# Performance work log

Measured on AMD Instinct MI355X. Metric: run time of the kernel, lower is better.

Reference implementation:

```python
import jax, jax.numpy as jnp
import numpy as np

N_NODES = 100_000
N_EDGES = 3_200_000
HIDDEN = 16


def setup_inputs() -> dict:
    key = jax.random.key(0)
    k1, k2, k3, k4 = jax.random.split(key, 4)
    x = jax.random.normal(k1, (N_NODES, 3), dtype=jnp.float32)
    edge_index = jax.random.randint(k2, (2, N_EDGES), 0, N_NODES, dtype=jnp.int32)
    # Glorot-style init for the two GCN layers (PyG GCNConv: lin weight + bias)
    W1 = jax.random.normal(k3, (3, HIDDEN), dtype=jnp.float32) * (1.0 / np.sqrt(3.0))
    b1 = jnp.zeros((HIDDEN,), dtype=jnp.float32)
    W2 = jax.random.normal(k4, (HIDDEN, 1), dtype=jnp.float32) * (1.0 / np.sqrt(HIDDEN))
    b2 = jnp.zeros((1,), dtype=jnp.float32)
    return {"x": x, "edge_index": edge_index, "W1": W1, "b1": b1, "W2": W2, "b2": b2}


def reference(x, edge_index, W1, b1, W2, b2):
    n = x.shape[0]  # static under jit
    # GCNConv default: add self-loops, symmetric degree normalization
    self_loop = jnp.arange(n, dtype=edge_index.dtype)
    src = jnp.concatenate([edge_index[0], self_loop])
    dst = jnp.concatenate([edge_index[1], self_loop])
    deg = jax.ops.segment_sum(jnp.ones_like(src, dtype=x.dtype), dst, num_segments=n)
    inv_sqrt_deg = jnp.where(deg > 0, jax.lax.rsqrt(jnp.maximum(deg, 1.0)), 0.0)
    norm = inv_sqrt_deg[src] * inv_sqrt_deg[dst]  # [E+N]

    def gcn_conv(h, W, b):
        h = h @ W  # linear transform first (cheaper: small out dim)
        msg = norm[:, None] * h[src]  # gather + scale
        return jax.ops.segment_sum(msg, dst, num_segments=n) + b  # scatter-add

    h = jax.nn.relu(gcn_conv(x, W1, b1))
    out = gcn_conv(h, W2, b2)
    return out.squeeze(-1)  # [N]
```

## Files before the change

### kernel.cpp

```cpp
#include <hip/hip_runtime.h>

#define HIDDEN 16
#define FB 128
#define FB_SHIFT 7
#define NBK_MAX 4096
#define FCHUNK 8192
#define FTH 512
#define CB 1024
#define CB_SHIFT 10
#define NCB_MAX 512
#define CHUNK 4096
#define SPL 8
#define BT 1024


__global__ __launch_bounds__(FTH) void
k_histf(const int* __restrict__ dst, int e, int nbk, int nchunk,
        unsigned int* __restrict__ hcT) {
    __shared__ unsigned int h[NBK_MAX];
    for (int i = threadIdx.x; i < nbk; i += FTH) h[i] = 0u;
    __syncthreads();
    int start = blockIdx.x * FCHUNK;
    int end = min(start + FCHUNK, e);
    for (int i = start + threadIdx.x; i < end; i += FTH)
        atomicAdd(&h[((unsigned)dst[i]) >> FB_SHIFT], 1u);
    __syncthreads();
    for (int j = threadIdx.x; j < nbk; j += FTH)
        hcT[(size_t)j * nchunk + blockIdx.x] = h[j];
}

__global__ void k_scanf(unsigned int* __restrict__ hcT,
                        unsigned int* __restrict__ cntc, int nchunk) {
    __shared__ unsigned int ts[256];
    __shared__ unsigned int carry;
    int b = blockIdx.x, t = threadIdx.x;
    if (t == 0) carry = 0u;
    __syncthreads();
    size_t row = (size_t)b * nchunk;
    for (int t0 = 0; t0 < nchunk; t0 += 256) {
        int i = t0 + t;
        unsigned int v = (i < nchunk) ? hcT[row + i] : 0u;
        ts[t] = v;
        __syncthreads();
        for (int off = 1; off < 256; off <<= 1) {
            unsigned int u = (t >= off) ? ts[t - off] : 0u;
            __syncthreads();
            ts[t] += u;
            __syncthreads();
        }
        if (i < nchunk) hcT[row + i] = carry + ts[t] - v;
        __syncthreads();
        if (t == 0) carry += ts[255];
        __syncthreads();
    }
    if (t == 0) cntc[b] = carry;
}

__global__ __launch_bounds__(1024) void
k_scanb(const unsigned int* __restrict__ cntc, int nbk,
        unsigned int* __restrict__ basec,
        unsigned int* __restrict__ rowptr, int n, unsigned int e) {
    __shared__ unsigned int tsum[1024];
    int t = threadIdx.x;
    int K = (nbk + 1023) / 1024;
    unsigned int s = 0;
    for (int k = 0; k < K; k++) {
        int i = t * K + k;
        if (i < nbk) s += cntc[i];
    }
    tsum[t] = s;
    __syncthreads();
    for (int off = 1; off < 1024; off <<= 1) {
        unsigned int v = (t >= off) ? tsum[t - off] : 0u;
        __syncthreads();
        tsum[t] += v;
        __syncthreads();
    }
    unsigned int run = (t == 0) ? 0u : tsum[t - 1];
    for (int k = 0; k < K; k++) {
        int i = t * K + k;
        if (i < nbk) { basec[i] = run; run += cntc[i]; }
    }
    if (t == 1023) basec[nbk] = tsum[1023];
    if (t == 0) rowptr[n] = e;
}

__global__ __launch_bounds__(FTH) void
k_fillf(const int* __restrict__ src, const int* __restrict__ dst,
        int e, int nbk, int nchunk,
        const unsigned int* __restrict__ basec,
        const unsigned int* __restrict__ hcT,
        unsigned int* __restrict__ tmp) {
    __shared__ unsigned int h[NBK_MAX];
    __shared__ unsigned int lb[NBK_MAX];
    for (int j = threadIdx.x; j < nbk; j += FTH) {
        lb[j] = basec[j] + hcT[(size_t)j * nchunk + blockIdx.x];
        h[j] = 0u;
    }
    __syncthreads();
    int start = blockIdx.x * FCHUNK;
    int end = min(start + FCHUNK, e);
    for (int i = start + threadIdx.x; i < end; i += FTH) {
        unsigned int d = (unsigned)dst[i];
        unsigned int s = (unsigned)src[i];
        unsigned int b = d >> FB_SHIFT;
        unsigned int r = atomicAdd(&h[b], 1u);
        tmp[lb[b] + r] = (s << FB_SHIFT) | (d & (FB - 1u));
    }
}

__global__ __launch_bounds__(256) void
k_sortN(const unsigned int* __restrict__ tmp,
        const unsigned int* __restrict__ basec,
        const float* __restrict__ x,
        unsigned int* __restrict__ rowptr, unsigned int* __restrict__ tmp2,
        float4* __restrict__ xs4, int n) {
    __shared__ unsigned int cnt[FB];
    __shared__ unsigned int sc[FB];
    __shared__ unsigned int cur[FB];
    int t = threadIdx.x, b = blockIdx.x;
    unsigned int s = basec[b], endp = basec[b + 1];
    if (t < FB) cnt[t] = 0u;
    __syncthreads();
    for (unsigned int i = s + t; i < endp; i += 256)
        atomicAdd(&cnt[tmp[i] & (FB - 1u)], 1u);
    __syncthreads();
    if (t < FB) sc[t] = cnt[t];
    __syncthreads();
    for (int off = 1; off < FB; off <<= 1) {
        unsigned int v = (t < FB && t >= off) ? sc[t - off] : 0u;
        __syncthreads();
        if (t < FB && t >= off) sc[t] += v;
        __syncthreads();
    }
    if (t < FB) {
        unsigned int excl = sc[t] - cnt[t];
        cur[t] = s + excl;
        int node = (b << FB_SHIFT) + t;
        if (node < n) {
            rowptr[node] = s + excl;
            float iv = rsqrtf((float)(1u + cnt[t]));
            xs4[node] = make_float4(x[3 * node] * iv, x[3 * node + 1] * iv,
                                    x[3 * node + 2] * iv, iv);
        }
    }
    __syncthreads();
    for (unsigned int i = s + t; i < endp; i += 256) {
        unsigned int rec = tmp[i];
        unsigned int r = atomicAdd(&cur[rec & (FB - 1u)], 1u);
        tmp2[r] = rec >> FB_SHIFT;
    }
}

__global__ void k_s1(const unsigned int* __restrict__ rowptr,
                     const unsigned int* __restrict__ tmp2,
                     const float4* __restrict__ xs4,
                     const float* __restrict__ W1, const float* __restrict__ b1,
                     const float* __restrict__ W2, const float* __restrict__ b2,
                     float* __restrict__ t2s, float* __restrict__ out, int n) {
    int gid = blockIdx.x * blockDim.x + threadIdx.x;
    int i = gid >> 1, h = gid & 1;
    bool valid = (i < n);
    unsigned int s = 0, epos = 0;
    if (valid) { s = rowptr[i]; epos = rowptr[i + 1]; }
    unsigned int half = (epos - s) >> 1;
    unsigned int b0 = h ? s + half : s;
    unsigned int b1r = h ? epos : s + half;
    float v0 = 0.f, v1 = 0.f, v2 = 0.f;
    unsigned int j = b0;
    for (; j + 4 <= b1r; j += 4) {
        unsigned a0 = tmp2[j], a1 = tmp2[j + 1], a2 = tmp2[j + 2], a3 = tmp2[j + 3];
        float4 p0 = xs4[a0], p1 = xs4[a1], p2 = xs4[a2], p3 = xs4[a3];
        v0 += (p0.x + p1.x) + (p2.x + p3.x);
        v1 += (p0.y + p1.y) + (p2.y + p3.y);
        v2 += (p0.z + p1.z) + (p2.z + p3.z);
    }
    for (; j < b1r; j++) {
        float4 p = xs4[tmp2[j]];
        v0 += p.x; v1 += p.y; v2 += p.z;
    }
    v0 += __shfl_xor(v0, 1);
    v1 += __shfl_xor(v1, 1);
    v2 += __shfl_xor(v2, 1);
    if (valid && h == 0) {
        float4 me = xs4[i];
        float iv = me.w;
        v0 = (v0 + me.x) * iv;
        v1 = (v1 + me.y) * iv;
        v2 = (v2 + me.z) * iv;
        float acc = 0.f;
#pragma unroll
        for (int k = 0; k < HIDDEN; k++) {
            float hh = fmaxf(fmaf(v0, W1[k], fmaf(v1, W1[HIDDEN + k],
                            fmaf(v2, W1[2 * HIDDEN + k], b1[k]))), 0.f);
            acc += hh * W2[k];
        }
        t2s[i] = acc * iv;
        out[i] = b2[0] + acc * iv * iv;
    }
}

__global__ void k_s2(const unsigned int* __restrict__ rowptr,
                     const unsigned int* __restrict__ tmp2,
                     const float* __restrict__ t2s, const float4* __restrict__ xs4,
                     float* __restrict__ out, int n) {
    int gid = blockIdx.x * blockDim.x + threadIdx.x;
    int i = gid >> 1, h = gid & 1;
    bool valid = (i < n);
    unsigned int s = 0, epos = 0;
    if (valid) { s = rowptr[i]; epos = rowptr[i + 1]; }
    unsigned int half = (epos - s) >> 1;
    unsigned int b0 = h ? s + half : s;
    unsigned int b1r = h ? epos : s + half;
    float v = 0.f;
    unsigned int j = b0;
    for (; j + 4 <= b1r; j += 4) {
        unsigned a0 = tmp2[j], a1 = tmp2[j + 1], a2 = tmp2[j + 2], a3 = tmp2[j + 3];
        v += (t2s[a0] + t2s[a1]) + (t2s[a2] + t2s[a3]);
    }
    for (; j < b1r; j++) v += t2s[tmp2[j]];
    v += __shfl_xor(v, 1);
    if (valid && h == 0) out[i] += v * xs4[i].w;
}


__global__ void k_zero(unsigned int* a, int na) {
    int i = blockIdx.x * blockDim.x + threadIdx.x;
    if (i < na) a[i] = 0u;
}
__global__ void k_hist_c(const int* __restrict__ dst, int e, int ncb, int nchunk,
                         unsigned int* __restrict__ cntc,
                         unsigned int* __restrict__ hcT) {
    __shared__ unsigned int h[NCB_MAX];
    for (int i = threadIdx.x; i < ncb; i += blockDim.x) h[i] = 0u;
    __syncthreads();
    int start = blockIdx.x * CHUNK;
    int end = min(start + CHUNK, e);
    for (int i = start + threadIdx.x; i < end; i += 256)
        atomicAdd(&h[((unsigned)dst[i]) >> CB_SHIFT], 1u);
    __syncthreads();
    for (int j = threadIdx.x; j < ncb; j += blockDim.x) {
        hcT[(size_t)j * nchunk + blockIdx.x] = h[j];
        if (h[j]) atomicAdd(&cntc[j], h[j]);
    }
}
__global__ void k_scan(const unsigned int* __restrict__ cnt, int nb,
                       unsigned int* __restrict__ base) {
    __shared__ unsigned int tsum[256];
    int t = threadIdx.x;
    int K = (nb + 255) / 256;
    unsigned int s = 0;
    for (int k = 0; k < K; k++) {
        int i = t * K + k;
        if (i < nb) s += cnt[i];
    }
    tsum[t] = s;
    __syncthreads();
    for (int off = 1; off < 256; off <<= 1) {
        unsigned int v = (t >= off) ? tsum[t - off] : 0u;
        __syncthreads();
        tsum[t] += v;
        __syncthreads();
    }
    unsigned int run = (t == 0) ? 0u : tsum[t - 1];
    for (int k = 0; k < K; k++) {
        int i = t * K + k;
        if (i < nb) { base[i] = run; run += cnt[i]; }
    }
}
__global__ void k_scanc(const unsigned int* __restrict__ hcT,
                        const unsigned int* __restrict__ basec,
                        unsigned int* __restrict__ lbasec, int nchunk) {
    __shared__ unsigned int ts[256];
    __shared__ unsigned int carry;
    int b = blockIdx.x, t = threadIdx.x;
    if (t == 0) carry = basec[b];
    __syncthreads();
    for (int t0 = 0; t0 < nchunk; t0 += 256) {
        int i = t0 + t;
        unsigned int v = (i < nchunk) ? hcT[(size_t)b * nchunk + i] : 0u;
        ts[t] = v;
        __syncthreads();
        for (int off = 1; off < 256; off <<= 1) {
            unsigned int u = (t >= off) ? ts[t - off] : 0u;
            __syncthreads();
            ts[t] += u;
            __syncthreads();
        }
        if (i < nchunk) lbasec[(size_t)b * nchunk + i] = carry + ts[t] - v;
        __syncthreads();
        if (t == 0) carry += ts[255];
        __syncthreads();
    }
}
__global__ void k_fill_c(const int* __restrict__ src, const int* __restrict__ dst,
                         int e, int ncb, int nchunk,
                         const unsigned int* __restrict__ lbasec,
                         unsigned int* __restrict__ tmp) {
    __shared__ unsigned int h[NCB_MAX];
    __shared__ unsigned int lb[NCB_MAX];
    for (int j = threadIdx.x; j < ncb; j += blockDim.x) {
        lb[j] = lbasec[(size_t)j * nchunk + blockIdx.x];
        h[j] = 0u;
    }
    __syncthreads();
    int start = blockIdx.x * CHUNK;
    int end = min(start + CHUNK, e);
    for (int i = start + threadIdx.x; i < end; i += 256) {
        unsigned int d = (unsigned)dst[i];
        unsigned int b = d >> CB_SHIFT;
        unsigned int r = atomicAdd(&h[b], 1u);
        tmp[lb[b] + r] = (((unsigned)src[i]) << CB_SHIFT) | (d & (CB - 1u));
    }
}
__global__ __launch_bounds__(BT) void
k_deg_split(const unsigned int* __restrict__ tmp, const unsigned int* __restrict__ basec,
            const unsigned int* __restrict__ cntc, unsigned int* __restrict__ deg, int n) {
    __shared__ unsigned int degl[CB];
    int t = threadIdx.x;
    degl[t] = 0u;
    __syncthreads();
    int b = blockIdx.x / SPL, sl = blockIdx.x % SPL;
    unsigned int s = basec[b], m = cntc[b];
    for (unsigned int i = sl * BT + t; i < m; i += SPL * BT)
        atomicAdd(&degl[tmp[s + i] & (CB - 1u)], 1u);
    __syncthreads();
    int node = b * CB + t;
    unsigned int c = degl[t];
    if (node < n && c) atomicAdd(&deg[node], c);
}
__global__ void k_inv_s(const unsigned int* __restrict__ deg, const float* __restrict__ x,
                        float4* __restrict__ xs4, int n) {
    int i = blockIdx.x * blockDim.x + threadIdx.x;
    if (i >= n) return;
    float iv = rsqrtf((float)(deg[i] + 1u));
    xs4[i] = make_float4(x[3 * i] * iv, x[3 * i + 1] * iv, x[3 * i + 2] * iv, iv);
}
__global__ __launch_bounds__(BT) void
k_s1_split(const unsigned int* __restrict__ tmp, const unsigned int* __restrict__ basec,
           const unsigned int* __restrict__ cntc, const float4* __restrict__ xs4,
           float* __restrict__ agg0, float* __restrict__ agg1, float* __restrict__ agg2, int n) {
    __shared__ float a0[CB], a1[CB], a2[CB];
    int t = threadIdx.x;
    a0[t] = 0.f; a1[t] = 0.f; a2[t] = 0.f;
    __syncthreads();
    int b = blockIdx.x / SPL, sl = blockIdx.x % SPL;
    unsigned int s = basec[b], m = cntc[b];
    for (unsigned int i = sl * BT + t; i < m; i += SPL * BT) {
        unsigned rec = tmp[s + i];
        float4 v = xs4[rec >> CB_SHIFT];
        unsigned dl = rec & (CB - 1u);
        atomicAdd(&a0[dl], v.x); atomicAdd(&a1[dl], v.y); atomicAdd(&a2[dl], v.z);
    }
    __syncthreads();
    int node = b * CB + t;
    if (node < n) {
        if (a0[t] != 0.f) atomicAdd(&agg0[node], a0[t]);
        if (a1[t] != 0.f) atomicAdd(&agg1[node], a1[t]);
        if (a2[t] != 0.f) atomicAdd(&agg2[node], a2[t]);
    }
}
__global__ void k_epi_s(const float* __restrict__ agg0, const float* __restrict__ agg1,
                        const float* __restrict__ agg2, const float4* __restrict__ xs4,
                        const float* __restrict__ W1, const float* __restrict__ b1,
                        const float* __restrict__ W2, const float* __restrict__ b2,
                        float* __restrict__ t2s, float* __restrict__ out, int n) {
    int i = blockIdx.x * blockDim.x + threadIdx.x;
    if (i >= n) return;
    float4 xv = xs4[i];
    float iv = xv.w;
    float v0 = iv * (agg0[i] + xv.x), v1 = iv * (agg1[i] + xv.y), v2 = iv * (agg2[i] + xv.z);
    float acc = 0.f;
#pragma unroll
    for (int j = 0; j < HIDDEN; j++) {
        float h = fmaxf(fmaf(v0, W1[j], fmaf(v1, W1[HIDDEN + j],
                       fmaf(v2, W1[2 * HIDDEN + j], b1[j]))), 0.f);
        acc += h * W2[j];
    }
    t2s[i] = acc * iv;
    out[i] = b2[0] + acc * iv * iv;
}
__global__ __launch_bounds__(BT) void
k_s2_split(const unsigned int* __restrict__ tmp, const unsigned int* __restrict__ basec,
           const unsigned int* __restrict__ cntc, const float* __restrict__ t2s,
           const float4* __restrict__ xs4, float* __restrict__ out, int n) {
    __shared__ float o[CB];
    int t = threadIdx.x;
    o[t] = 0.f;
    __syncthreads();
    int b = blockIdx.x / SPL, sl = blockIdx.x % SPL;
    unsigned int s = basec[b], m = cntc[b];
    for (unsigned int i = sl * BT + t; i < m; i += SPL * BT) {
        unsigned rec = tmp[s + i];
        atomicAdd(&o[rec & (CB - 1u)], t2s[rec >> CB_SHIFT]);
    }
    __syncthreads();
    int node = b * CB + t;
    if (node < n && o[t] != 0.f) atomicAdd(&out[node], o[t] * xs4[node].w);
}


extern "C" void kernel_launch(void* const* d_in, const int* in_sizes, int n_in,
                              void* d_out, int out_size, void* d_ws, size_t ws_size,
                              hipStream_t stream) {
    const float* x  = (const float*)d_in[0];
    const int*   ei = (const int*)d_in[1];
    const float* W1 = (const float*)d_in[2];
    const float* b1 = (const float*)d_in[3];
    const float* W2 = (const float*)d_in[4];
    const float* b2 = (const float*)d_in[5];
    float* out = (float*)d_out;

    int n = in_sizes[0] / 3;
    int e = in_sizes[1] / 2;
    const int* src = ei;
    const int* dst = ei + e;
    const int B = 256;

    int nbk = (n + FB - 1) / FB;
    int nchunkf = (e + FCHUNK - 1) / FCHUNK;
    int gridN2 = (2 * n + B - 1) / B;

    size_t needf = (size_t)n * 16 + (size_t)n * 4 + (size_t)(n + 1) * 4
                 + (size_t)(2 * nbk + 1) * 4 + (size_t)nbk * nchunkf * 4
                 + (size_t)e * 8 + 64;

    if (nbk <= NBK_MAX && n < (1 << 25) && ws_size >= needf) {
        float4* xs4 = (float4*)d_ws;
        float* t2s = (float*)(xs4 + n);
        unsigned int* rowptr = (unsigned int*)(t2s + n);
        unsigned int* cntc   = rowptr + (n + 1);
        unsigned int* basec  = cntc + nbk;
        unsigned int* hcT    = basec + nbk + 1;
        unsigned int* tmp    = hcT + (size_t)nbk * nchunkf;
        unsigned int* tmp2   = tmp + e;

        k_histf<<<nchunkf, FTH, 0, stream>>>(dst, e, nbk, nchunkf, hcT);
        k_scanf<<<nbk, 256, 0, stream>>>(hcT, cntc, nchunkf);
        k_scanb<<<1, 1024, 0, stream>>>(cntc, nbk, basec, rowptr, n, (unsigned)e);
        k_fillf<<<nchunkf, FTH, 0, stream>>>(src, dst, e, nbk, nchunkf, basec, hcT, tmp);
        k_sortN<<<nbk, 256, 0, stream>>>(tmp, basec, x, rowptr, tmp2, xs4, n);
        k_s1<<<gridN2, B, 0, stream>>>(rowptr, tmp2, xs4, W1, b1, W2, b2, t2s, out, n);
        k_s2<<<gridN2, B, 0, stream>>>(rowptr, tmp2, t2s, xs4, out, n);
    } else {
        int ncb = (n + CB - 1) / CB;
        int gridE = (e + CHUNK - 1) / CHUNK;
        int gridN = (n + B - 1) / B;
        float4* xs4 = (float4*)d_ws;
        float* agg0 = (float*)(xs4 + n);
        float* agg1 = agg0 + n;
        float* agg2 = agg1 + n;
        unsigned int* deg = (unsigned int*)(agg2 + n);
        float* t2s = (float*)(deg + n);
        unsigned int* cntc   = (unsigned int*)(t2s + n);
        unsigned int* basec  = cntc + ncb;
        unsigned int* hcT    = basec + ncb;
        unsigned int* lbasec = hcT + (size_t)ncb * gridE;
        unsigned int* tmp    = lbasec + (size_t)ncb * gridE;

        k_zero<<<(4 * n + ncb + B - 1) / B, B, 0, stream>>>((unsigned int*)agg0, 4 * n);
        k_zero<<<(ncb + B - 1) / B, B, 0, stream>>>(cntc, ncb);
        k_hist_c<<<gridE, B, 0, stream>>>(dst, e, ncb, gridE, cntc, hcT);
        k_scan<<<1, B, 0, stream>>>(cntc, ncb, basec);
        k_scanc<<<ncb, B, 0, stream>>>(hcT, basec, lbasec, gridE);
        k_fill_c<<<gridE, B, 0, stream>>>(src, dst, e, ncb, gridE, lbasec, tmp);
        k_deg_split<<<ncb * SPL, BT, 0, stream>>>(tmp, basec, cntc, deg, n);
        k_inv_s<<<gridN, B, 0, stream>>>(deg, x, xs4, n);
        k_s1_split<<<ncb * SPL, BT, 0, stream>>>(tmp, basec, cntc, xs4, agg0, agg1, agg2, n);
        k_epi_s<<<gridN, B, 0, stream>>>(agg0, agg1, agg2, xs4, W1, b1, W2, b2, t2s, out, n);
        k_s2_split<<<ncb * SPL, BT, 0, stream>>>(tmp, basec, cntc, t2s, xs4, out, n);
    }
}
```

Baseline: 190.3 us.

## Use coarser 512-node buckets and reorder global scan in CSR build

Coarse bucket size grows from 128 to 512 nodes, cutting the bucket count and with it the per-chunk histogram matrix, the scan work and the shared-memory footprint of the histogram and fill kernels. Bucket totals are now gathered with global atomics during the histogram pass, so the global scan runs before the per-bucket chunk scan, which writes into a separate lbasec array. The histogram loop is also unrolled four ways. The trade-off is an extra zeroing launch, more work per bucket in the local sort (512 threads, longer scan), and fewer source bits left in the packed record (the node limit drops to 2^23).

Result: slower. 195.3 us (+2.6%).

```diff
diff --git a/kernel.cpp b/kernel.cpp
--- a/kernel.cpp
+++ b/kernel.cpp
@@ -1,11 +1,11 @@
 #include <hip/hip_runtime.h>
 
 #define HIDDEN 16
-#define FB 128
-#define FB_SHIFT 7
-#define NBK_MAX 4096
-#define FCHUNK 8192
-#define FTH 512
+#define MB 512
+#define MB_SHIFT 9
+#define NMB_MAX 1024
+#define MCHUNK 8192
+#define MTH 512
 #define CB 1024
 #define CB_SHIFT 10
 #define NCB_MAX 512
@@ -14,32 +14,76 @@
 #define BT 1024
 
 
-__global__ __launch_bounds__(FTH) void
-k_histf(const int* __restrict__ dst, int e, int nbk, int nchunk,
-        unsigned int* __restrict__ hcT) {
-    __shared__ unsigned int h[NBK_MAX];
-    for (int i = threadIdx.x; i < nbk; i += FTH) h[i] = 0u;
-    __syncthreads();
-    int start = blockIdx.x * FCHUNK;
-    int end = min(start + FCHUNK, e);
-    for (int i = start + threadIdx.x; i < end; i += FTH)
-        atomicAdd(&h[((unsigned)dst[i]) >> FB_SHIFT], 1u);
-    __syncthreads();
-    for (int j = threadIdx.x; j < nbk; j += FTH)
+__global__ void k_zerom(unsigned int* cntc, int nmb) {
+    int i = blockIdx.x * blockDim.x + threadIdx.x;
+    if (i < nmb) cntc[i] = 0u;
+}
+
+__global__ __launch_bounds__(MTH) void
+k_histm(const int* __restrict__ dst, int e, int nmb, int nchunk,
+        unsigned int* __restrict__ cntc, unsigned int* __restrict__ hcT) {
+    __shared__ unsigned int h[NMB_MAX];
+    for (int i = threadIdx.x; i < nmb; i += MTH) h[i] = 0u;
+    __syncthreads();
+    int start = blockIdx.x * MCHUNK;
+    int end = min(start + MCHUNK, e);
+    int i = start + threadIdx.x;
+    for (; i + 3 * MTH < end; i += 4 * MTH) {
+        unsigned d0 = dst[i], d1 = dst[i + MTH], d2 = dst[i + 2 * MTH], d3 = dst[i + 3 * MTH];
+        atomicAdd(&h[d0 >> MB_SHIFT], 1u);
+        atomicAdd(&h[d1 >> MB_SHIFT], 1u);
+        atomicAdd(&h[d2 >> MB_SHIFT], 1u);
+        atomicAdd(&h[d3 >> MB_SHIFT], 1u);
+    }
+    for (; i < end; i += MTH)
+        atomicAdd(&h[((unsigned)dst[i]) >> MB_SHIFT], 1u);
+    __syncthreads();
+    for (int j = threadIdx.x; j < nmb; j += MTH) {
         hcT[(size_t)j * nchunk + blockIdx.x] = h[j];
-}
-
-__global__ void k_scanf(unsigned int* __restrict__ hcT,
-                        unsigned int* __restrict__ cntc, int nchunk) {
+        if (h[j]) atomicAdd(&cntc[j], h[j]);
+    }
+}
+
+__global__ __launch_bounds__(1024) void
+k_scanm(const unsigned int* __restrict__ cntc, int nmb,
+        unsigned int* __restrict__ basec,
+        unsigned int* __restrict__ rowptr, int n, unsigned int e) {
+    __shared__ unsigned int tsum[1024];
+    int t = threadIdx.x;
+    int K = (nmb + 1023) / 1024;
+    unsigned int s = 0;
+    for (int k = 0; k < K; k++) {
+        int i = t * K + k;
+        if (i < nmb) s += cntc[i];
+    }
+    tsum[t] = s;
+    __syncthreads();
+    for (int off = 1; off < 1024; off <<= 1) {
+        unsigned int v = (t >= off) ? tsum[t - off] : 0u;
+        __syncthreads();
+        tsum[t] += v;
+        __syncthreads();
+    }
+    unsigned int run = (t == 0) ? 0u : tsum[t - 1];
+    for (int k = 0; k < K; k++) {
+        int i = t * K + k;
+        if (i < nmb) { basec[i] = run; run += cntc[i]; }
+    }
+    if (t == 1023) basec[nmb] = tsum[1023];
+    if (t == 0) rowptr[n] = e;
+}
+
+__global__ void k_scancm(const unsigned int* __restrict__ hcT,
+                         const unsigned int* __restrict__ basec,
+                         unsigned int* __restrict__ lbasec, int nchunk) {
     __shared__ unsigned int ts[256];
     __shared__ unsigned int carry;
     int b = blockIdx.x, t = threadIdx.x;
-    if (t == 0) carry = 0u;
-    __syncthreads();
-    size_t row = (size_t)b * nchunk;
+    if (t == 0) carry = basec[b];
+    __syncthreads();
     for (int t0 = 0; t0 < nchunk; t0 += 256) {
         int i = t0 + t;
-        unsigned int v = (i < nchunk) ? hcT[row + i] : 0u;
+        unsigned int v = (i < nchunk) ? hcT[(size_t)b * nchunk + i] : 0u;
         ts[t] = v;
         __syncthreads();
         for (int off = 1; off < 256; off <<= 1) {
@@ -48,107 +92,74 @@
             ts[t] += u;
             __syncthreads();
         }
-        if (i < nchunk) hcT[row + i] = carry + ts[t] - v;
+        if (i < nchunk) lbasec[(size_t)b * nchunk + i] = carry + ts[t] - v;
         __syncthreads();
         if (t == 0) carry += ts[255];
         __syncthreads();
     }
-    if (t == 0) cntc[b] = carry;
-}
-
-__global__ __launch_bounds__(1024) void
-k_scanb(const unsigned int* __restrict__ cntc, int nbk,
-        unsigned int* __restrict__ basec,
-        unsigned int* __restrict__ rowptr, int n, unsigned int e) {
-    __shared__ unsigned int tsum[1024];
-    int t = threadIdx.x;
-    int K = (nbk + 1023) / 1024;
-    unsigned int s = 0;
-    for (int k = 0; k < K; k++) {
-        int i = t * K + k;
-        if (i < nbk) s += cntc[i];
-    }
-    tsum[t] = s;
-    __syncthreads();
-    for (int off = 1; off < 1024; off <<= 1) {
-        unsigned int v = (t >= off) ? tsum[t - off] : 0u;
-        __syncthreads();
-        tsum[t] += v;
-        __syncthreads();
-    }
-    unsigned int run = (t == 0) ? 0u : tsum[t - 1];
-    for (int k = 0; k < K; k++) {
-        int i = t * K + k;
-        if (i < nbk) { basec[i] = run; run += cntc[i]; }
-    }
-    if (t == 1023) basec[nbk] = tsum[1023];
-    if (t == 0) rowptr[n] = e;
-}
-
-__global__ __launch_bounds__(FTH) void
-k_fillf(const int* __restrict__ src, const int* __restrict__ dst,
-        int e, int nbk, int nchunk,
-        const unsigned int* __restrict__ basec,
-        const unsigned int* __restrict__ hcT,
+}
+
+__global__ __launch_bounds__(MTH) void
+k_fillm(const int* __restrict__ src, const int* __restrict__ dst,
+        int e, int nmb, int nchunk,
+        const unsigned int* __restrict__ lbasec,
         unsigned int* __restrict__ tmp) {
-    __shared__ unsigned int h[NBK_MAX];
-    __shared__ unsigned int lb[NBK_MAX];
-    for (int j = threadIdx.x; j < nbk; j += FTH) {
-        lb[j] = basec[j] + hcT[(size_t)j * nchunk + blockIdx.x];
+    __shared__ unsigned int h[NMB_MAX];
+    __shared__ unsigned int lb[NMB_MAX];
+    for (int j = threadIdx.x; j < nmb; j += MTH) {
+        lb[j] = lbasec[(size_t)j * nchunk + blockIdx.x];
         h[j] = 0u;
     }
     __syncthreads();
-    int start = blockIdx.x * FCHUNK;
-    int end = min(start + FCHUNK, e);
-    for (int i = start + threadIdx.x; i < end; i += FTH) {
+    int start = blockIdx.x * MCHUNK;
+    int end = min(start + MCHUNK, e);
+    for (int i = start + threadIdx.x; i < end; i += MTH) {
         unsigned int d = (unsigned)dst[i];
         unsigned int s = (unsigned)src[i];
-        unsigned int b = d >> FB_SHIFT;
+        unsigned int b = d >> MB_SHIFT;
         unsigned int r = atomicAdd(&h[b], 1u);
-        tmp[lb[b] + r] = (s << FB_SHIFT) | (d & (FB - 1u));
-    }
-}
-
-__global__ __launch_bounds__(256) void
-k_sortN(const unsigned int* __restrict__ tmp,
+        tmp[lb[b] + r] = (s << MB_SHIFT) | (d & (MB - 1u));
+    }
+}
+
+__global__ __launch_bounds__(MB) void
+k_sortC(const unsigned int* __restrict__ tmp,
         const unsigned int* __restrict__ basec,
         const float* __restrict__ x,
         unsigned int* __restrict__ rowptr, unsigned int* __restrict__ tmp2,
         float4* __restrict__ xs4, int n) {
-    __shared__ unsigned int cnt[FB];
-    __shared__ unsigned int sc[FB];
-    __shared__ unsigned int cur[FB];
+    __shared__ unsigned int cnt[MB];
+    __shared__ unsigned int sc[MB];
+    __shared__ unsigned int cur[MB];
     int t = threadIdx.x, b = blockIdx.x;
     unsigned int s = basec[b], endp = basec[b + 1];
-    if (t < FB) cnt[t] = 0u;
-    __syncthreads();
-    for (unsigned int i = s + t; i < endp; i += 256)
-        atomicAdd(&cnt[tmp[i] & (FB - 1u)], 1u);
-    __syncthreads();
-    if (t < FB) sc[t] = cnt[t];
-    __syncthreads();
-    for (int off = 1; off < FB; off <<= 1) {
-        unsigned int v = (t < FB && t >= off) ? sc[t - off] : 0u;
-        __syncthreads();
-        if (t < FB && t >= off) sc[t] += v;
-        __syncthreads();
-    }
-    if (t < FB) {
-        unsigned int excl = sc[t] - cnt[t];
-        cur[t] = s + excl;
-        int node = (b << FB_SHIFT) + t;
-        if (node < n) {
-            rowptr[node] = s + excl;
-            float iv = rsqrtf((float)(1u + cnt[t]));
-            xs4[node] = make_float4(x[3 * node] * iv, x[3 * node + 1] * iv,
-                                    x[3 * node + 2] * iv, iv);
-        }
-    }
-    __syncthreads();
-    for (unsigned int i = s + t; i < endp; i += 256) {
+    cnt[t] = 0u;
+    __syncthreads();
+    for (unsigned int i = s + t; i < endp; i += MB)
+        atomicAdd(&cnt[tmp[i] & (MB - 1u)], 1u);
+    __syncthreads();
+    sc[t] = cnt[t];
+    __syncthreads();
+    for (int off = 1; off < MB; off <<= 1) {
+        unsigned int v = (t >= off) ? sc[t - off] : 0u;
+        __syncthreads();
+        sc[t] += v;
+        __syncthreads();
+    }
+    unsigned int excl = sc[t] - cnt[t];
+    cur[t] = s + excl;
+    int node = (b << MB_SHIFT) + t;
+    if (node < n) {
+        rowptr[node] = s + excl;
+        float iv = rsqrtf((float)(1u + cnt[t]));
+        xs4[node] = make_float4(x[3 * node] * iv, x[3 * node + 1] * iv,
+                                x[3 * node + 2] * iv, iv);
+    }
+    __syncthreads();
+    for (unsigned int i = s + t; i < endp; i += MB) {
         unsigned int rec = tmp[i];
-        unsigned int r = atomicAdd(&cur[rec & (FB - 1u)], 1u);
-        tmp2[r] = rec >> FB_SHIFT;
+        unsigned int r = atomicAdd(&cur[rec & (MB - 1u)], 1u);
+        tmp2[r] = rec >> MB_SHIFT;
     }
 }
 
@@ -417,29 +428,31 @@
     const int* dst = ei + e;
     const int B = 256;
 
-    int nbk = (n + FB - 1) / FB;
-    int nchunkf = (e + FCHUNK - 1) / FCHUNK;
+    int nmb = (n + MB - 1) / MB;
+    int nchunkm = (e + MCHUNK - 1) / MCHUNK;
     int gridN2 = (2 * n + B - 1) / B;
 
-    size_t needf = (size_t)n * 16 + (size_t)n * 4 + (size_t)(n + 1) * 4
-                 + (size_t)(2 * nbk + 1) * 4 + (size_t)nbk * nchunkf * 4
+    size_t needm = (size_t)n * 16 + (size_t)n * 4 + (size_t)(n + 1) * 4
+                 + (size_t)(2 * nmb + 1) * 4 + (size_t)nmb * nchunkm * 8
                  + (size_t)e * 8 + 64;
 
-    if (nbk <= NBK_MAX && n < (1 << 25) && ws_size >= needf) {
+    if (nmb <= NMB_MAX && n < (1 << 23) && ws_size >= needm) {
         float4* xs4 = (float4*)d_ws;
         float* t2s = (float*)(xs4 + n);
         unsigned int* rowptr = (unsigned int*)(t2s + n);
         unsigned int* cntc   = rowptr + (n + 1);
-        unsigned int* basec  = cntc + nbk;
-        unsigned int* hcT    = basec + nbk + 1;
-        unsigned int* tmp    = hcT + (size_t)nbk * nchunkf;
+        unsigned int* basec  = cntc + nmb;
+        unsigned int* hcT    = basec + nmb + 1;
+        unsigned int* lbasec = hcT + (size_t)nmb * nchunkm;
+        unsigned int* tmp    = lbasec + (size_t)nmb * nchunkm;
         unsigned int* tmp2   = tmp + e;
 
-        k_histf<<<nchunkf, FTH, 0, stream>>>(dst, e, nbk, nchunkf, hcT);
-        k_scanf<<<nbk, 256, 0, stream>>>(hcT, cntc, nchunkf);
-        k_scanb<<<1, 1024, 0, stream>>>(cntc, nbk, basec, rowptr, n, (unsigned)e);
-        k_fillf<<<nchunkf, FTH, 0, stream>>>(src, dst, e, nbk, nchunkf, basec, hcT, tmp);
-        k_sortN<<<nbk, 256, 0, stream>>>(tmp, basec, x, rowptr, tmp2, xs4, n);
+        k_zerom<<<(nmb + B - 1) / B, B, 0, stream>>>(cntc, nmb);
+        k_histm<<<nchunkm, MTH, 0, stream>>>(dst, e, nmb, nchunkm, cntc, hcT);
+        k_scanm<<<1, 1024, 0, stream>>>(cntc, nmb, basec, rowptr, n, (unsigned)e);
+        k_scancm<<<nmb, 256, 0, stream>>>(hcT, basec, lbasec, nchunkm);
+        k_fillm<<<nchunkm, MTH, 0, stream>>>(src, dst, e, nmb, nchunkm, lbasec, tmp);
+        k_sortC<<<nmb, MB, 0, stream>>>(tmp, basec, x, rowptr, tmp2, xs4, n);
         k_s1<<<gridN2, B, 0, stream>>>(rowptr, tmp2, xs4, W1, b1, W2, b2, t2s, out, n);
         k_s2<<<gridN2, B, 0, stream>>>(rowptr, tmp2, t2s, xs4, out, n);
     } else {
```
